# Performance work log

Measured on AMD Instinct MI355X. Metric: run time of the kernel, lower is better.

The kernel has to match this reference:

```python
import jax, jax.numpy as jnp
import numpy as np

T = 32          # n_node_types
EXTRA = 3       # input_dim = T + 3
D = 9           # perfect binary tree depth -> N = 2**D - 1 = 511 nodes/plan
N = 2 ** D - 1
EMB = 64
HID = 64
FC = 64
OUT = 8         # N_METRICS
NS = 5          # N_SAMPLES
P = 2560        # number of plans (P // NS = 512 groups)
B = 512


def setup_inputs() -> dict:
    key = jax.random.key(0)
    ks = jax.random.split(key, 8)

    def lin(k, o, i):
        return (jax.random.normal(k, (o, i), jnp.float32) / np.sqrt(i)).astype(jnp.float32)

    x0 = jax.random.normal(ks[0], (P, N, T + EXTRA), jnp.float32)
    x = jax.random.uniform(ks[1], (B, P // NS), jnp.float32)
    return {
        "x": x,
        "x0": x0,
        "W_emb": lin(ks[2], EMB, T), "b_emb": jnp.zeros((EMB,), jnp.float32),
        "W0": lin(ks[3], HID, EMB + EXTRA), "b0": jnp.zeros((HID,), jnp.float32),
        "W1": lin(ks[4], HID, EMB + EXTRA + 2 * HID), "b1": jnp.zeros((HID,), jnp.float32),
        "Wfc1": lin(ks[5], FC, HID), "bfc1": jnp.zeros((FC,), jnp.float32),
        "Wfc2": lin(ks[6], OUT, FC), "bfc2": jnp.zeros((OUT,), jnp.float32),
    }


def reference(x, x0, W_emb, b_emb, W0, b0, W1, b1, Wfc1, bfc1, Wfc2, bfc2):
    # --- enc_dnn: per-node embed + concat(extra, children hiddens) + Linear + ReLU ---
    # node_emb = emb(xi[:T]); node_input = [node_emb, xi[T:], h_children...]
    emb = jnp.einsum('pnt,et->pne', x0[..., :T], W_emb) + b_emb    # [P,N,EMB]
    feats = jnp.concatenate([emb, x0[..., T:]], axis=-1)           # [P,N,EMB+3]
    # heap layout: node i's children are 2i+1, 2i+2; level l occupies [2^l-1, 2^{l+1}-1)
    lo = 2 ** (D - 1) - 1
    h = jax.nn.relu(jnp.einsum('pnf,hf->pnh', feats[:, lo:], W0) + b0)  # leaves
    for l in range(D - 2, -1, -1):  # structural loop over tree levels (fixed, small)
        lo, n = 2 ** l - 1, 2 ** l
        f = feats[:, lo:lo + n]
        inp = jnp.concatenate([f, h[:, 0::2], h[:, 1::2]], axis=-1)  # [emb|extra|h_left|h_right]
        h = jax.nn.relu(jnp.einsum('pnf,hf->pnh', inp, W1) + b1)
    h0 = h[:, 0]                                                   # root hidden, [P,HID]
    # --- agg_weight ---
    mean_h = h0.reshape(-1, NS, HID).mean(axis=1)                  # [P/NS, HID]
    weighted = x @ mean_h                                          # [B, HID]
    hid = jax.nn.relu(weighted @ Wfc1.T + bfc1)
    return hid @ Wfc2.T + bfc2                                     # [B, OUT]
```

## Files before the change

kernel.cpp:

```cpp
#include <hip/hip_runtime.h>
#include <hip/hip_bf16.h>


typedef __attribute__((ext_vector_type(8))) short s8v;
typedef __attribute__((ext_vector_type(4))) float f4v;
typedef unsigned short u16;
typedef unsigned int   u32;

__device__ __forceinline__ u16 f2bf(float f) {
    return __builtin_bit_cast(u16, __float2bfloat16(f));
}
__device__ __forceinline__ f4v mfma16(s8v a, s8v b, f4v c) {
    return __builtin_amdgcn_mfma_f32_16x16x32_bf16(a, b, c, 0, 0, 0);
}
#define SWZ(r) ((((r) & 1) | (((r) >> 1) & 6)) << 3)

__device__ __forceinline__ u32 pk2(float a, float b) {
    return (u32)f2bf(fmaxf(a, 0.f)) | ((u32)f2bf(fmaxf(b, 0.f)) << 16);
}
__device__ __forceinline__ s8v pkfrag(f4v h0, f4v h1) {
    int4 d;
    d.x = (int)pk2(h0[0], h0[1]); d.y = (int)pk2(h0[2], h0[3]);
    d.z = (int)pk2(h1[0], h1[1]); d.w = (int)pk2(h1[2], h1[3]);
    return __builtin_bit_cast(s8v, d);
}
__device__ __forceinline__ s8v xB0(const float* __restrict__ xr, int lq) {
    float4 A = *(const float4*)(xr + lq * 8);
    float4 B = *(const float4*)(xr + lq * 8 + 4);
    s8v r;
    r[0]=(short)f2bf(A.x); r[1]=(short)f2bf(A.y); r[2]=(short)f2bf(A.z); r[3]=(short)f2bf(A.w);
    r[4]=(short)f2bf(B.x); r[5]=(short)f2bf(B.y); r[6]=(short)f2bf(B.z); r[7]=(short)f2bf(B.w);
    return r;
}
__device__ __forceinline__ s8v xB1(const float* __restrict__ xr, int lq) {
    s8v r = (s8v){0,0,0,0,0,0,0,0};
    if (lq == 0) {
        float4 T = *(const float4*)(xr + 31);
        r[0]=(short)f2bf(T.y); r[1]=(short)f2bf(T.z); r[2]=(short)f2bf(T.w);
    }
    return r;
}
__device__ __forceinline__ s8v wread(const u16* w, int stride, int row, int ks, int lq) {
    return *(const s8v*)(w + row * stride + ks * 32 + lq * 8);
}
__device__ __forceinline__ f4v bias4(const float* __restrict__ b) {
    float4 t = *(const float4*)b; return (f4v){t.x, t.y, t.z, t.w};
}
__device__ __forceinline__ int sigp(int rho, int s, int h) {
    return 32*s + 4*h + ((rho & 12) << 1) + (rho & 3);
}

__global__ void prep_kernel(const float* __restrict__ W_emb, const float* __restrict__ b_emb,
                            const float* __restrict__ W0, const float* __restrict__ b0,
                            const float* __restrict__ W1, const float* __restrict__ b1,
                            u16* __restrict__ wt1, u16* __restrict__ wt0,
                            float* __restrict__ b1p, float* __restrict__ b0p)
{
    int idx = blockIdx.x * 256 + threadIdx.x;
    if (idx < 64 * 192) {
        int h = idx / 192, k = idx % 192;
        float v;
        if (k < 32) { v = 0.f; for (int e = 0; e < 64; e++) v = fmaf(W1[h*195+e], W_emb[e*32+k], v); }
        else if (k < 35)  v = W1[h*195 + 64 + (k - 32)];
        else if (k < 64)  v = 0.f;
        else              v = W1[h*195 + 67 + (k - 64)];
        wt1[h*192 + k] = f2bf(v);
    } else if (idx < 64*192 + 64*64) {
        int j = idx - 64*192; int h = j >> 6, k = j & 63;
        float v;
        if (k < 32)      { v = 0.f; for (int e = 0; e < 64; e++) v = fmaf(W0[h*67+e], W_emb[e*32+k], v); }
        else if (k < 35)   v = W0[h*67 + 64 + (k - 32)];
        else               v = 0.f;
        wt0[h*64 + k] = f2bf(v);
    } else if (idx < 64*192 + 64*64 + 64) {
        int h = idx - (64*192 + 64*64);
        float v = b1[h];
        for (int e = 0; e < 64; e++) v = fmaf(W1[h*195+e], b_emb[e], v);
        b1p[h] = v;
    } else if (idx < 64*192 + 64*64 + 128) {
        int h = idx - (64*192 + 64*64 + 64);
        float v = b0[h];
        for (int e = 0; e < 64; e++) v = fmaf(W0[h*67+e], b_emb[e], v);
        b0p[h] = v;
    }
}

__global__ __launch_bounds__(512, 2) void tree_all(
    const float* __restrict__ x0,
    const u16* __restrict__ wt1g, const u16* __restrict__ wt0g,
    const float* __restrict__ b1p, const float* __restrict__ b0p,
    float* __restrict__ h0out)
{
    __shared__ __align__(16) u16 wt1s[64 * 200];
    __shared__ __align__(16) u16 wt0s[64 * 40 + 64];
    __shared__ __align__(16) u16 buf6[4 * 64 * 64];

    const int tid = threadIdx.x;
    const int l   = tid & 63;
    const int w   = tid >> 6;
    const int lq  = l >> 4;
    const int rho = l & 15;
    const int pair = w >> 2;
    const int c    = w & 3;
    const int tA = blockIdx.x * 4 + 2 * pair;
    const int tB = tA + 1;
    const float* xbA = x0 + (size_t)tA * 511 * 35;
    const float* xbB = x0 + (size_t)tB * 511 * 35;

    {
        u32* d1 = (u32*)wt1s; const u32* s1 = (const u32*)wt1g;
        #pragma unroll
        for (int t = 0; t < 12; t++) {
            int i = t*512 + tid;
            int row = i / 96, kk = i - row*96;
            d1[row*100 + kk] = s1[row*96 + kk];
        }
        u32* d0 = (u32*)wt0s; const u32* s0 = (const u32*)wt0g;
        #pragma unroll
        for (int t = 0; t < 3; t++) {
            int i = t*512 + tid;
            if (i < 1280) { int row = i / 20, kk = i - row*20; d0[row*20 + kk] = s0[row*32 + kk]; }
        }
        if (tid < 32) ((u32*)(wt0s + 64*40))[tid] = 0;
    }
    __syncthreads();

    s8v TLA[4][2], TLB[4][2];
    {
        s8v WL[4][2]; f4v bL[4];
        #pragma unroll
        for (int i = 0; i < 4; i++) {
            int sg = sigp(rho, i >> 1, i & 1);
            WL[i][0] = wread(wt0s, 40, sg, 0, lq);
            WL[i][1] = wread(wt0s, 40, sg, 1, lq);
            bL[i] = bias4(b0p + 32*(i>>1) + 8*lq + 4*(i&1));
        }
        #pragma unroll
        for (int q = 0; q < 4; q++) {
            const float* xrA = xbA + (size_t)(255 + 64*c + 4*rho + q) * 35;
            const float* xrB = xbB + (size_t)(255 + 64*c + 4*rho + q) * 35;
            s8v xaA = xB0(xrA, lq), xtA = xB1(xrA, lq);
            s8v xaB = xB0(xrB, lq), xtB = xB1(xrB, lq);
            f4v aA[4], aB[4];
            #pragma unroll
            for (int i = 0; i < 4; i++) { aA[i] = bL[i]; aB[i] = bL[i]; }
            #pragma unroll
            for (int i = 0; i < 4; i++) {
                aA[i] = mfma16(WL[i][0], xaA, aA[i]);
                aA[i] = mfma16(WL[i][1], xtA, aA[i]);
                aB[i] = mfma16(WL[i][0], xaB, aB[i]);
                aB[i] = mfma16(WL[i][1], xtB, aB[i]);
            }
            TLA[q][0] = pkfrag(aA[0], aA[1]); TLA[q][1] = pkfrag(aA[2], aA[3]);
            TLB[q][0] = pkfrag(aB[0], aB[1]); TLB[q][1] = pkfrag(aB[2], aB[3]);
        }
    }

    s8v A7[4], B7[4];
    {
        f4v aAE[4], aAO[4], aBE[4], aBO[4];
        #pragma unroll
        for (int i = 0; i < 4; i++) {
            f4v b = bias4(b1p + 32*(i>>1) + 8*lq + 4*(i&1));
            aAE[i] = b; aAO[i] = b; aBE[i] = b; aBO[i] = b;
        }
        {
            const float* xrAE = xbA + (size_t)(127 + 32*c + 2*rho) * 35;
            const float* xrBE = xbB + (size_t)(127 + 32*c + 2*rho) * 35;
            s8v xAE0 = xB0(xrAE, lq),      xAE1 = xB1(xrAE, lq);
            s8v xAO0 = xB0(xrAE + 35, lq), xAO1 = xB1(xrAE + 35, lq);
            s8v xBE0 = xB0(xrBE, lq),      xBE1 = xB1(xrBE, lq);
            s8v xBO0 = xB0(xrBE + 35, lq), xBO1 = xB1(xrBE + 35, lq);
            #pragma unroll
            for (int i = 0; i < 4; i++) {
                int sg = sigp(rho, i >> 1, i & 1);
                s8v w0 = wread(wt1s, 200, sg, 0, lq);
                s8v w1 = wread(wt1s, 200, sg, 1, lq);
                aAE[i] = mfma16(w0, xAE0, aAE[i]); aAE[i] = mfma16(w1, xAE1, aAE[i]);
                aAO[i] = mfma16(w0, xAO0, aAO[i]); aAO[i] = mfma16(w1, xAO1, aAO[i]);
                aBE[i] = mfma16(w0, xBE0, aBE[i]); aBE[i] = mfma16(w1, xBE1, aBE[i]);
                aBO[i] = mfma16(w0, xBO0, aBO[i]); aBO[i] = mfma16(w1, xBO1, aBO[i]);
            }
        }
        #pragma unroll
        for (int i = 0; i < 4; i++) {
            int sg = sigp(rho, i >> 1, i & 1);
            s8v w2 = wread(wt1s, 200, sg, 2, lq);
            s8v w3 = wread(wt1s, 200, sg, 3, lq);
            s8v w4 = wread(wt1s, 200, sg, 4, lq);
            s8v w5 = wread(wt1s, 200, sg, 5, lq);
            aAE[i] = mfma16(w2, TLA[0][0], aAE[i]); aAE[i] = mfma16(w3, TLA[0][1], aAE[i]);
            aAE[i] = mfma16(w4, TLA[1][0], aAE[i]); aAE[i] = mfma16(w5, TLA[1][1], aAE[i]);
            aAO[i] = mfma16(w2, TLA[2][0], aAO[i]); aAO[i] = mfma16(w3, TLA[2][1], aAO[i]);
            aAO[i] = mfma16(w4, TLA[3][0], aAO[i]); aAO[i] = mfma16(w5, TLA[3][1], aAO[i]);
            aBE[i] = mfma16(w2, TLB[0][0], aBE[i]); aBE[i] = mfma16(w3, TLB[0][1], aBE[i]);
            aBE[i] = mfma16(w4, TLB[1][0], aBE[i]); aBE[i] = mfma16(w5, TLB[1][1], aBE[i]);
            aBO[i] = mfma16(w2, TLB[2][0], aBO[i]); aBO[i] = mfma16(w3, TLB[2][1], aBO[i]);
            aBO[i] = mfma16(w4, TLB[3][0], aBO[i]); aBO[i] = mfma16(w5, TLB[3][1], aBO[i]);
        }
        A7[0] = pkfrag(aAE[0], aAE[1]); A7[1] = pkfrag(aAE[2], aAE[3]);
        A7[2] = pkfrag(aAO[0], aAO[1]); A7[3] = pkfrag(aAO[2], aAO[3]);
        B7[0] = pkfrag(aBE[0], aBE[1]); B7[1] = pkfrag(aBE[2], aBE[3]);
        B7[2] = pkfrag(aBO[0], aBO[1]); B7[3] = pkfrag(aBO[2], aBO[3]);
    }

    {
        const float* xrA6 = xbA + (size_t)(63 + 16*c + rho) * 35;
        const float* xrB6 = xbB + (size_t)(63 + 16*c + rho) * 35;
        s8v xA0 = xB0(xrA6, lq), xA1 = xB1(xrA6, lq);
        s8v xBv0 = xB0(xrB6, lq), xBv1 = xB1(xrB6, lq);
        u16* slA = buf6 + (2*pair) * 4096;
        u16* slB = slA + 4096;
        int r6 = 16*c + rho;
        int sw6 = SWZ(r6);
        #pragma unroll
        for (int cc = 0; cc < 4; cc++) {
            int sg = 16*cc + rho;
            s8v w0 = wread(wt1s, 200, sg, 0, lq);
            s8v w1 = wread(wt1s, 200, sg, 1, lq);
            s8v w2 = wread(wt1s, 200, sg, 2, lq);
            s8v w3 = wread(wt1s, 200, sg, 3, lq);
            s8v w4 = wread(wt1s, 200, sg, 4, lq);
            s8v w5 = wread(wt1s, 200, sg, 5, lq);
            f4v bb = bias4(b1p + 16*cc + 4*lq);
            f4v aA = bb, aB = bb;
            aA = mfma16(w0, xA0, aA);  aA = mfma16(w1, xA1, aA);
            aA = mfma16(w2, A7[0], aA); aA = mfma16(w3, A7[1], aA);
            aA = mfma16(w4, A7[2], aA); aA = mfma16(w5, A7[3], aA);
            aB = mfma16(w0, xBv0, aB); aB = mfma16(w1, xBv1, aB);
            aB = mfma16(w2, B7[0], aB); aB = mfma16(w3, B7[1], aB);
            aB = mfma16(w4, B7[2], aB); aB = mfma16(w5, B7[3], aB);
            int col = (16*cc + 4*lq) ^ sw6;
            uint2 dA; dA.x = pk2(aA[0], aA[1]); dA.y = pk2(aA[2], aA[3]);
            uint2 dB; dB.x = pk2(aB[0], aB[1]); dB.y = pk2(aB[2], aB[3]);
            *(uint2*)(slA + (size_t)r6 * 64 + col) = dA;
            *(uint2*)(slB + (size_t)r6 * 64 + col) = dB;
        }
    }
    __syncthreads();

    if (w < 4) {
        const int tree = blockIdx.x * 4 + w;
        u16* slice = buf6 + w * 4096;
        const float* xb = x0 + (size_t)tree * 511 * 35;

        s8v ch5[2][2][2];
        #pragma unroll
        for (int d5 = 0; d5 < 2; d5++)
        #pragma unroll
        for (int pr = 0; pr < 2; pr++) {
            int row = 4*rho + 2*d5 + pr;
            int sw = SWZ(row);
            ch5[d5][pr][0] = *(const s8v*)(slice + (size_t)row*64 + ((     8*lq) ^ sw));
            ch5[d5][pr][1] = *(const s8v*)(slice + (size_t)row*64 + ((32 + 8*lq) ^ sw));
        }
        const float* xr5E = xb + (size_t)(31 + 2*rho) * 35;
        s8v x5E0 = xB0(xr5E, lq),      x5E1 = xB1(xr5E, lq);
        s8v x5O0 = xB0(xr5E + 35, lq), x5O1 = xB1(xr5E + 35, lq);
        f4v aE[4], aO[4];
        #pragma unroll
        for (int i = 0; i < 4; i++) {
            f4v b = bias4(b1p + 32*(i>>1) + 8*lq + 4*(i&1));
            aE[i] = b; aO[i] = b;
        }
        #pragma unroll
        for (int i = 0; i < 4; i++) {
            int sg = sigp(rho, i >> 1, i & 1);
            s8v w0 = wread(wt1s, 200, sg, 0, lq);
            s8v w1 = wread(wt1s, 200, sg, 1, lq);
            s8v w2 = wread(wt1s, 200, sg, 2, lq);
            s8v w3 = wread(wt1s, 200, sg, 3, lq);
            s8v w4 = wread(wt1s, 200, sg, 4, lq);
            s8v w5 = wread(wt1s, 200, sg, 5, lq);
            aE[i] = mfma16(w0, x5E0, aE[i]); aE[i] = mfma16(w1, x5E1, aE[i]);
            aE[i] = mfma16(w2, ch5[0][0][0], aE[i]); aE[i] = mfma16(w3, ch5[0][0][1], aE[i]);
            aE[i] = mfma16(w4, ch5[0][1][0], aE[i]); aE[i] = mfma16(w5, ch5[0][1][1], aE[i]);
            aO[i] = mfma16(w0, x5O0, aO[i]); aO[i] = mfma16(w1, x5O1, aO[i]);
            aO[i] = mfma16(w2, ch5[1][0][0], aO[i]); aO[i] = mfma16(w3, ch5[1][0][1], aO[i]);
            aO[i] = mfma16(w4, ch5[1][1][0], aO[i]); aO[i] = mfma16(w5, ch5[1][1][1], aO[i]);
        }
        s8v L5E0 = pkfrag(aE[0], aE[1]), L5E1 = pkfrag(aE[2], aE[3]);
        s8v L5O0 = pkfrag(aO[0], aO[1]), L5O1 = pkfrag(aO[2], aO[3]);

        {
            const float* xr4 = xb + (size_t)(15 + rho) * 35;
            s8v x40 = xB0(xr4, lq), x41 = xB1(xr4, lq);
            int sw4 = SWZ(rho);
            #pragma unroll
            for (int cc = 0; cc < 4; cc++) {
                int sg = 16*cc + rho;
                s8v w0 = wread(wt1s, 200, sg, 0, lq);
                s8v w1 = wread(wt1s, 200, sg, 1, lq);
                s8v w2 = wread(wt1s, 200, sg, 2, lq);
                s8v w3 = wread(wt1s, 200, sg, 3, lq);
                s8v w4 = wread(wt1s, 200, sg, 4, lq);
                s8v w5 = wread(wt1s, 200, sg, 5, lq);
                f4v a = bias4(b1p + 16*cc + 4*lq);
                a = mfma16(w0, x40, a);  a = mfma16(w1, x41, a);
                a = mfma16(w2, L5E0, a); a = mfma16(w3, L5E1, a);
                a = mfma16(w4, L5O0, a); a = mfma16(w5, L5O1, a);
                int col = (16*cc + 4*lq) ^ sw4;
                uint2 d; d.x = pk2(a[0], a[1]); d.y = pk2(a[2], a[3]);
                *(uint2*)(slice + (size_t)rho * 64 + col) = d;
            }
        }
        asm volatile("s_waitcnt lgkmcnt(0)" ::: "memory");

        u16* tb0 = slice + 32 * 64;
        u16* tb1 = slice;
        float bv[4];
        #pragma unroll
        for (int ct = 0; ct < 4; ct++) bv[ct] = b1p[ct*16 + rho];
        f4v acc[4];

        auto tlevel = [&](int lo, const u16* cb) {
            const float* xr = xb + (size_t)(lo + rho) * 35;
            s8v a0 = xB0(xr, lq), a1 = xB1(xr, lq);
            #pragma unroll
            for (int ct = 0; ct < 4; ct++) acc[ct] = (f4v){bv[ct], bv[ct], bv[ct], bv[ct]};
            #pragma unroll
            for (int ct = 0; ct < 4; ct++) {
                acc[ct] = mfma16(a0, wread(wt1s, 200, ct*16 + rho, 0, lq), acc[ct]);
                acc[ct] = mfma16(a1, wread(wt1s, 200, ct*16 + rho, 1, lq), acc[ct]);
            }
            #pragma unroll
            for (int ks = 0; ks < 4; ks++) {
                int k0 = ks*32 + lq*8;
                int rr = 2*rho + (k0 >> 6);
                s8v ach = *(const s8v*)(cb + (size_t)rr*64 + ((k0 & 63) ^ SWZ(rr)));
                #pragma unroll
                for (int ct = 0; ct < 4; ct++)
                    acc[ct] = mfma16(ach, wread(wt1s, 200, ct*16 + rho, 2 + ks, lq), acc[ct]);
            }
        };
        auto tstore = [&](u16* buf) {
            #pragma unroll
            for (int r = 0; r < 4; r++) {
                int ro = lq*4 + r; int sw = SWZ(ro);
                #pragma unroll
                for (int ct = 0; ct < 4; ct++)
                    buf[ro*64 + ((ct*16 + rho) ^ sw)] = f2bf(fmaxf(acc[ct][r], 0.f));
            }
            asm volatile("s_waitcnt lgkmcnt(0)" ::: "memory");
        };

        tlevel(7, slice);  tstore(tb0);
        tlevel(3, tb0);    tstore(tb1);
        tlevel(1, tb1);    tstore(tb0);
        tlevel(0, tb0);
        if (lq == 0) {
            #pragma unroll
            for (int ct = 0; ct < 4; ct++)
                h0out[(size_t)tree*64 + ct*16 + rho] = fmaxf(acc[ct][0], 0.f);
        }
    }
}

__global__ void mean_kernel(const float* __restrict__ h0, float* __restrict__ mh)
{
    int idx = blockIdx.x * blockDim.x + threadIdx.x;
    if (idx < 512 * 64) {
        int g = idx >> 6, h = idx & 63;
        float s = 0.f;
        #pragma unroll
        for (int q = 0; q < 5; q++) s += h0[(size_t)(g * 5 + q) * 64 + h];
        mh[idx] = s * 0.2f;
    }
}

__global__ __launch_bounds__(64) void head_kernel(const float* __restrict__ x,
                                                  const float* __restrict__ mh,
                                                  const float* __restrict__ Wfc1,
                                                  const float* __restrict__ bfc1,
                                                  const float* __restrict__ Wfc2,
                                                  const float* __restrict__ bfc2,
                                                  float* __restrict__ out)
{
    __shared__ float sw[64];
    __shared__ float sh[64];
    int b = blockIdx.x, h = threadIdx.x;

    float a0 = 0.f, a1 = 0.f, a2 = 0.f, a3 = 0.f;
    const float* xr = x + (size_t)b * 512;
    for (int g = 0; g < 512; g += 4) {
        a0 = fmaf(xr[g + 0], mh[(g + 0) * 64 + h], a0);
        a1 = fmaf(xr[g + 1], mh[(g + 1) * 64 + h], a1);
        a2 = fmaf(xr[g + 2], mh[(g + 2) * 64 + h], a2);
        a3 = fmaf(xr[g + 3], mh[(g + 3) * 64 + h], a3);
    }
    sw[h] = (a0 + a1) + (a2 + a3);
    __syncthreads();

    float acc = bfc1[h];
    #pragma unroll 8
    for (int k = 0; k < 64; k++) acc = fmaf(Wfc1[h * 64 + k], sw[k], acc);
    sh[h] = fmaxf(acc, 0.f);
    __syncthreads();

    if (h < 8) {
        float o = bfc2[h];
        #pragma unroll 8
        for (int f = 0; f < 64; f++) o = fmaf(Wfc2[h * 64 + f], sh[f], o);
        out[(size_t)b * 8 + h] = o;
    }
}

extern "C" void kernel_launch(void* const* d_in, const int* in_sizes, int n_in,
                              void* d_out, int out_size, void* d_ws, size_t ws_size,
                              hipStream_t stream)
{
    (void)in_sizes; (void)n_in; (void)out_size; (void)ws_size;
    const float* x     = (const float*)d_in[0];
    const float* x0    = (const float*)d_in[1];
    const float* W_emb = (const float*)d_in[2];
    const float* b_emb = (const float*)d_in[3];
    const float* W0    = (const float*)d_in[4];
    const float* b0    = (const float*)d_in[5];
    const float* W1    = (const float*)d_in[6];
    const float* b1    = (const float*)d_in[7];
    const float* Wfc1  = (const float*)d_in[8];
    const float* bfc1  = (const float*)d_in[9];
    const float* Wfc2  = (const float*)d_in[10];
    const float* bfc2  = (const float*)d_in[11];
    float* out = (float*)d_out;

    u16* wt1   = (u16*)d_ws;
    u16* wt0   = wt1 + 64 * 192;
    float* b1p = (float*)(wt0 + 64 * 64);
    float* b0p = b1p + 64;
    float* h0  = b0p + 64;
    float* mh  = h0 + 2560 * 64;

    prep_kernel<<<65, 256, 0, stream>>>(W_emb, b_emb, W0, b0, W1, b1, wt1, wt0, b1p, b0p);
    tree_all<<<640, 512, 0, stream>>>(x0, wt1, wt0, b1p, b0p, h0);
    mean_kernel<<<128, 256, 0, stream>>>(h0, mh);
    head_kernel<<<512, 64, 0, stream>>>(x, mh, Wfc1, bfc1, Wfc2, bfc2, out);
}
```

Measured before the change: 88.57 us.

## Split level-5 tree work across all eight waves and prefetch first leaf inputs

Level 5 used to run on four of the eight waves, each doing both even and odd children. Now all eight waves take part: waves 4-7 compute the odd children and pass the packed results to waves 0-3 through shared memory, with two extra block barriers around the handoff. Separately, the first leaf rows' global loads are issued before the weight copy into shared memory, so their latency overlaps that copy. The rest of the upper levels still runs on four waves. The extra barriers and LDS traffic may cancel part of the gain from splitting the work.

```diff
diff --git a/kernel.cpp b/kernel.cpp
--- a/kernel.cpp
+++ b/kernel.cpp
@@ -24,13 +24,19 @@
     d.z = (int)pk2(h1[0], h1[1]); d.w = (int)pk2(h1[2], h1[3]);
     return __builtin_bit_cast(s8v, d);
 }
-__device__ __forceinline__ s8v xB0(const float* __restrict__ xr, int lq) {
-    float4 A = *(const float4*)(xr + lq * 8);
-    float4 B = *(const float4*)(xr + lq * 8 + 4);
+__device__ __forceinline__ s8v mkB0(float4 A, float4 B) {
     s8v r;
     r[0]=(short)f2bf(A.x); r[1]=(short)f2bf(A.y); r[2]=(short)f2bf(A.z); r[3]=(short)f2bf(A.w);
     r[4]=(short)f2bf(B.x); r[5]=(short)f2bf(B.y); r[6]=(short)f2bf(B.z); r[7]=(short)f2bf(B.w);
     return r;
+}
+__device__ __forceinline__ s8v mkB1(float4 T) {
+    s8v r = (s8v){0,0,0,0,0,0,0,0};
+    r[0]=(short)f2bf(T.y); r[1]=(short)f2bf(T.z); r[2]=(short)f2bf(T.w);
+    return r;
+}
+__device__ __forceinline__ s8v xB0(const float* __restrict__ xr, int lq) {
+    return mkB0(*(const float4*)(xr + lq * 8), *(const float4*)(xr + lq * 8 + 4));
 }
 __device__ __forceinline__ s8v xB1(const float* __restrict__ xr, int lq) {
     s8v r = (s8v){0,0,0,0,0,0,0,0};
@@ -107,6 +113,15 @@
     const float* xbA = x0 + (size_t)tA * 511 * 35;
     const float* xbB = x0 + (size_t)tB * 511 * 35;
 
+    const float* xq0A = xbA + (size_t)(255 + 64*c + 4*rho) * 35;
+    const float* xq0B = xbB + (size_t)(255 + 64*c + 4*rho) * 35;
+    float4 pAa = *(const float4*)(xq0A + lq*8);
+    float4 pAb = *(const float4*)(xq0A + lq*8 + 4);
+    float4 pAt = (lq == 0) ? *(const float4*)(xq0A + 31) : float4{0.f,0.f,0.f,0.f};
+    float4 pBa = *(const float4*)(xq0B + lq*8);
+    float4 pBb = *(const float4*)(xq0B + lq*8 + 4);
+    float4 pBt = (lq == 0) ? *(const float4*)(xq0B + 31) : float4{0.f,0.f,0.f,0.f};
+
     {
         u32* d1 = (u32*)wt1s; const u32* s1 = (const u32*)wt1g;
         #pragma unroll
@@ -135,12 +150,7 @@
             WL[i][1] = wread(wt0s, 40, sg, 1, lq);
             bL[i] = bias4(b0p + 32*(i>>1) + 8*lq + 4*(i&1));
         }
-        #pragma unroll
-        for (int q = 0; q < 4; q++) {
-            const float* xrA = xbA + (size_t)(255 + 64*c + 4*rho + q) * 35;
-            const float* xrB = xbB + (size_t)(255 + 64*c + 4*rho + q) * 35;
-            s8v xaA = xB0(xrA, lq), xtA = xB1(xrA, lq);
-            s8v xaB = xB0(xrB, lq), xtB = xB1(xrB, lq);
+        auto leafstep = [&](s8v xaA, s8v xtA, s8v xaB, s8v xtB, int q) {
             f4v aA[4], aB[4];
             #pragma unroll
             for (int i = 0; i < 4; i++) { aA[i] = bL[i]; aB[i] = bL[i]; }
@@ -153,6 +163,13 @@
             }
             TLA[q][0] = pkfrag(aA[0], aA[1]); TLA[q][1] = pkfrag(aA[2], aA[3]);
             TLB[q][0] = pkfrag(aB[0], aB[1]); TLB[q][1] = pkfrag(aB[2], aB[3]);
+        };
+        leafstep(mkB0(pAa, pAb), mkB1(pAt), mkB0(pBa, pBb), mkB1(pBt), 0);
+        #pragma unroll
+        for (int q = 1; q < 4; q++) {
+            const float* xrA = xbA + (size_t)(255 + 64*c + 4*rho + q) * 35;
+            const float* xrB = xbB + (size_t)(255 + 64*c + 4*rho + q) * 35;
+            leafstep(xB0(xrA, lq), xB1(xrA, lq), xB0(xrB, lq), xB1(xrB, lq), q);
         }
     }
 
@@ -239,30 +256,26 @@
     }
     __syncthreads();
 
-    if (w < 4) {
-        const int tree = blockIdx.x * 4 + w;
-        u16* slice = buf6 + w * 4096;
+    const int  tt   = w & 3;
+    const int  half = (w >= 4) ? 1 : 0;
+    {
+        const int tree = blockIdx.x * 4 + tt;
+        u16* slice = buf6 + tt * 4096;
         const float* xb = x0 + (size_t)tree * 511 * 35;
 
-        s8v ch5[2][2][2];
-        #pragma unroll
-        for (int d5 = 0; d5 < 2; d5++)
+        s8v ch5[2][2];
         #pragma unroll
         for (int pr = 0; pr < 2; pr++) {
-            int row = 4*rho + 2*d5 + pr;
+            int row = 4*rho + 2*half + pr;
             int sw = SWZ(row);
-            ch5[d5][pr][0] = *(const s8v*)(slice + (size_t)row*64 + ((     8*lq) ^ sw));
-            ch5[d5][pr][1] = *(const s8v*)(slice + (size_t)row*64 + ((32 + 8*lq) ^ sw));
-        }
-        const float* xr5E = xb + (size_t)(31 + 2*rho) * 35;
-        s8v x5E0 = xB0(xr5E, lq),      x5E1 = xB1(xr5E, lq);
-        s8v x5O0 = xB0(xr5E + 35, lq), x5O1 = xB1(xr5E + 35, lq);
-        f4v aE[4], aO[4];
-        #pragma unroll
-        for (int i = 0; i < 4; i++) {
-            f4v b = bias4(b1p + 32*(i>>1) + 8*lq + 4*(i&1));
-            aE[i] = b; aO[i] = b;
-        }
+            ch5[pr][0] = *(const s8v*)(slice + (size_t)row*64 + ((     8*lq) ^ sw));
+            ch5[pr][1] = *(const s8v*)(slice + (size_t)row*64 + ((32 + 8*lq) ^ sw));
+        }
+        const float* xr5 = xb + (size_t)(31 + 2*rho + half) * 35;
+        s8v x50 = xB0(xr5, lq), x51 = xB1(xr5, lq);
+        f4v a5[4];
+        #pragma unroll
+        for (int i = 0; i < 4; i++) a5[i] = bias4(b1p + 32*(i>>1) + 8*lq + 4*(i&1));
         #pragma unroll
         for (int i = 0; i < 4; i++) {
             int sg = sigp(rho, i >> 1, i & 1);
@@ -272,86 +285,95 @@
             s8v w3 = wread(wt1s, 200, sg, 3, lq);
             s8v w4 = wread(wt1s, 200, sg, 4, lq);
             s8v w5 = wread(wt1s, 200, sg, 5, lq);
-            aE[i] = mfma16(w0, x5E0, aE[i]); aE[i] = mfma16(w1, x5E1, aE[i]);
-            aE[i] = mfma16(w2, ch5[0][0][0], aE[i]); aE[i] = mfma16(w3, ch5[0][0][1], aE[i]);
-            aE[i] = mfma16(w4, ch5[0][1][0], aE[i]); aE[i] = mfma16(w5, ch5[0][1][1], aE[i]);
-            aO[i] = mfma16(w0, x5O0, aO[i]); aO[i] = mfma16(w1, x5O1, aO[i]);
-            aO[i] = mfma16(w2, ch5[1][0][0], aO[i]); aO[i] = mfma16(w3, ch5[1][0][1], aO[i]);
-            aO[i] = mfma16(w4, ch5[1][1][0], aO[i]); aO[i] = mfma16(w5, ch5[1][1][1], aO[i]);
-        }
-        s8v L5E0 = pkfrag(aE[0], aE[1]), L5E1 = pkfrag(aE[2], aE[3]);
-        s8v L5O0 = pkfrag(aO[0], aO[1]), L5O1 = pkfrag(aO[2], aO[3]);
-
-        {
-            const float* xr4 = xb + (size_t)(15 + rho) * 35;
-            s8v x40 = xB0(xr4, lq), x41 = xB1(xr4, lq);
-            int sw4 = SWZ(rho);
-            #pragma unroll
-            for (int cc = 0; cc < 4; cc++) {
-                int sg = 16*cc + rho;
-                s8v w0 = wread(wt1s, 200, sg, 0, lq);
-                s8v w1 = wread(wt1s, 200, sg, 1, lq);
-                s8v w2 = wread(wt1s, 200, sg, 2, lq);
-                s8v w3 = wread(wt1s, 200, sg, 3, lq);
-                s8v w4 = wread(wt1s, 200, sg, 4, lq);
-                s8v w5 = wread(wt1s, 200, sg, 5, lq);
-                f4v a = bias4(b1p + 16*cc + 4*lq);
-                a = mfma16(w0, x40, a);  a = mfma16(w1, x41, a);
-                a = mfma16(w2, L5E0, a); a = mfma16(w3, L5E1, a);
-                a = mfma16(w4, L5O0, a); a = mfma16(w5, L5O1, a);
-                int col = (16*cc + 4*lq) ^ sw4;
-                uint2 d; d.x = pk2(a[0], a[1]); d.y = pk2(a[2], a[3]);
-                *(uint2*)(slice + (size_t)rho * 64 + col) = d;
-            }
-        }
-        asm volatile("s_waitcnt lgkmcnt(0)" ::: "memory");
-
-        u16* tb0 = slice + 32 * 64;
-        u16* tb1 = slice;
-        float bv[4];
-        #pragma unroll
-        for (int ct = 0; ct < 4; ct++) bv[ct] = b1p[ct*16 + rho];
-        f4v acc[4];
-
-        auto tlevel = [&](int lo, const u16* cb) {
-            const float* xr = xb + (size_t)(lo + rho) * 35;
-            s8v a0 = xB0(xr, lq), a1 = xB1(xr, lq);
-            #pragma unroll
-            for (int ct = 0; ct < 4; ct++) acc[ct] = (f4v){bv[ct], bv[ct], bv[ct], bv[ct]};
-            #pragma unroll
-            for (int ct = 0; ct < 4; ct++) {
-                acc[ct] = mfma16(a0, wread(wt1s, 200, ct*16 + rho, 0, lq), acc[ct]);
-                acc[ct] = mfma16(a1, wread(wt1s, 200, ct*16 + rho, 1, lq), acc[ct]);
-            }
-            #pragma unroll
-            for (int ks = 0; ks < 4; ks++) {
-                int k0 = ks*32 + lq*8;
-                int rr = 2*rho + (k0 >> 6);
-                s8v ach = *(const s8v*)(cb + (size_t)rr*64 + ((k0 & 63) ^ SWZ(rr)));
-                #pragma unroll
-                for (int ct = 0; ct < 4; ct++)
-                    acc[ct] = mfma16(ach, wread(wt1s, 200, ct*16 + rho, 2 + ks, lq), acc[ct]);
-            }
-        };
-        auto tstore = [&](u16* buf) {
-            #pragma unroll
-            for (int r = 0; r < 4; r++) {
-                int ro = lq*4 + r; int sw = SWZ(ro);
-                #pragma unroll
-                for (int ct = 0; ct < 4; ct++)
-                    buf[ro*64 + ((ct*16 + rho) ^ sw)] = f2bf(fmaxf(acc[ct][r], 0.f));
+            a5[i] = mfma16(w0, x50, a5[i]);      a5[i] = mfma16(w1, x51, a5[i]);
+            a5[i] = mfma16(w2, ch5[0][0], a5[i]); a5[i] = mfma16(w3, ch5[0][1], a5[i]);
+            a5[i] = mfma16(w4, ch5[1][0], a5[i]); a5[i] = mfma16(w5, ch5[1][1], a5[i]);
+        }
+        s8v L5X0 = pkfrag(a5[0], a5[1]), L5X1 = pkfrag(a5[2], a5[3]);
+
+        __syncthreads();
+        if (half == 1) {
+            *(s8v*)(slice + 1024 + (size_t)l * 8) = L5X0;
+            *(s8v*)(slice + 1536 + (size_t)l * 8) = L5X1;
+        }
+        __syncthreads();
+
+        if (half == 0) {
+            s8v L5E0 = L5X0, L5E1 = L5X1;
+            s8v L5O0 = *(const s8v*)(slice + 1024 + (size_t)l * 8);
+            s8v L5O1 = *(const s8v*)(slice + 1536 + (size_t)l * 8);
+
+            {
+                const float* xr4 = xb + (size_t)(15 + rho) * 35;
+                s8v x40 = xB0(xr4, lq), x41 = xB1(xr4, lq);
+                int sw4 = SWZ(rho);
+                #pragma unroll
+                for (int cc = 0; cc < 4; cc++) {
+                    int sg = 16*cc + rho;
+                    s8v w0 = wread(wt1s, 200, sg, 0, lq);
+                    s8v w1 = wread(wt1s, 200, sg, 1, lq);
+                    s8v w2 = wread(wt1s, 200, sg, 2, lq);
+                    s8v w3 = wread(wt1s, 200, sg, 3, lq);
+                    s8v w4 = wread(wt1s, 200, sg, 4, lq);
+                    s8v w5 = wread(wt1s, 200, sg, 5, lq);
+                    f4v a = bias4(b1p + 16*cc + 4*lq);
+                    a = mfma16(w0, x40, a);  a = mfma16(w1, x41, a);
+                    a = mfma16(w2, L5E0, a); a = mfma16(w3, L5E1, a);
+                    a = mfma16(w4, L5O0, a); a = mfma16(w5, L5O1, a);
+                    int col = (16*cc + 4*lq) ^ sw4;
+                    uint2 d; d.x = pk2(a[0], a[1]); d.y = pk2(a[2], a[3]);
+                    *(uint2*)(slice + (size_t)rho * 64 + col) = d;
+                }
             }
             asm volatile("s_waitcnt lgkmcnt(0)" ::: "memory");
-        };
-
-        tlevel(7, slice);  tstore(tb0);
-        tlevel(3, tb0);    tstore(tb1);
-        tlevel(1, tb1);    tstore(tb0);
-        tlevel(0, tb0);
-        if (lq == 0) {
+
+            u16* tb0 = slice + 32 * 64;
+            u16* tb1 = slice;
+            float bv[4];
             #pragma unroll
-            for (int ct = 0; ct < 4; ct++)
-                h0out[(size_t)tree*64 + ct*16 + rho] = fmaxf(acc[ct][0], 0.f);
+            for (int ct = 0; ct < 4; ct++) bv[ct] = b1p[ct*16 + rho];
+            f4v acc[4];
+
+            auto tlevel = [&](int lo, const u16* cb) {
+                const float* xr = xb + (size_t)(lo + rho) * 35;
+                s8v a0 = xB0(xr, lq), a1 = xB1(xr, lq);
+                #pragma unroll
+                for (int ct = 0; ct < 4; ct++) acc[ct] = (f4v){bv[ct], bv[ct], bv[ct], bv[ct]};
+                #pragma unroll
+                for (int ct = 0; ct < 4; ct++) {
+                    acc[ct] = mfma16(a0, wread(wt1s, 200, ct*16 + rho, 0, lq), acc[ct]);
+                    acc[ct] = mfma16(a1, wread(wt1s, 200, ct*16 + rho, 1, lq), acc[ct]);
+                }
+                #pragma unroll
+                for (int ks = 0; ks < 4; ks++) {
+                    int k0 = ks*32 + lq*8;
+                    int rr = 2*rho + (k0 >> 6);
+                    s8v ach = *(const s8v*)(cb + (size_t)rr*64 + ((k0 & 63) ^ SWZ(rr)));
+                    #pragma unroll
+                    for (int ct = 0; ct < 4; ct++)
+                        acc[ct] = mfma16(ach, wread(wt1s, 200, ct*16 + rho, 2 + ks, lq), acc[ct]);
+                }
+            };
+            auto tstore = [&](u16* buf) {
+                #pragma unroll
+                for (int r = 0; r < 4; r++) {
+                    int ro = lq*4 + r; int sw = SWZ(ro);
+                    #pragma unroll
+                    for (int ct = 0; ct < 4; ct++)
+                        buf[ro*64 + ((ct*16 + rho) ^ sw)] = f2bf(fmaxf(acc[ct][r], 0.f));
+                }
+                asm volatile("s_waitcnt lgkmcnt(0)" ::: "memory");
+            };
+
+            tlevel(7, slice);  tstore(tb0);
+            tlevel(3, tb0);    tstore(tb1);
+            tlevel(1, tb1);    tstore(tb0);
+            tlevel(0, tb0);
+            if (lq == 0) {
+                #pragma unroll
+                for (int ct = 0; ct < 4; ct++)
+                    h0out[(size_t)tree*64 + ct*16 + rho] = fmaxf(acc[ct][0], 0.f);
+            }
         }
     }
 }
```

New measurement: 89.92 us. Within noise of the previous version (+1.5%).
